# Kernel tuning notes

Measured on AMD Instinct MI355X. Metric: run time of the kernel, lower is better.

Reference implementation:

```python
import jax, jax.numpy as jnp
import numpy as np

N = 200000          # nodes
E = 800000          # edges (avg degree ~4, molecular graphs)
F_IN = 128          # dataset.num_node_features
HID = 32            # hidden_channels -> widths 32, 64, 128
N_TASKS = 128       # dataset.num_tasks
G = 8000            # number of graphs in the batch
EPS = 1e-5


def _glorot(key, shape):
    fan_in, fan_out = shape[0], shape[1]
    lim = np.sqrt(6.0 / (fan_in + fan_out)).astype(np.float32)
    return jax.random.uniform(key, shape, jnp.float32, -lim, lim)


def setup_inputs() -> dict:
    key = jax.random.key(0)
    ks = jax.random.split(key, 16)
    x = jax.random.normal(ks[0], (N, F_IN), jnp.float32)
    edge_index = jax.random.randint(ks[1], (2, E), 0, N, jnp.int64)
    batch = jnp.sort(jax.random.randint(ks[2], (N,), 0, G, jnp.int64))
    return {
        "x": x,
        "edge_index": edge_index,
        "batch": batch,
        "norm_w": jnp.ones((1,), jnp.float32),
        "norm_b": jnp.zeros((1,), jnp.float32),
        "W1": _glorot(ks[3], (F_IN, HID)),
        "b1": jnp.zeros((HID,), jnp.float32),
        "W2": _glorot(ks[4], (HID, 2 * HID)),
        "b2": jnp.zeros((2 * HID,), jnp.float32),
        "W3": _glorot(ks[5], (2 * HID, 4 * HID)),
        "b3": jnp.zeros((4 * HID,), jnp.float32),
        "lin1_W": _glorot(ks[6], (4 * HID, 256)),
        "lin1_b": jnp.zeros((256,), jnp.float32),
        "lin2_W": _glorot(ks[7], (256, N_TASKS)),
        "lin2_b": jnp.zeros((N_TASKS,), jnp.float32),
    }


def _instance_norm(x, batch, w, b):
    # PyG InstanceNorm: per-graph, per-channel mean / biased var, scalar affine.
    ones = jnp.ones((x.shape[0], 1), x.dtype)
    cnt = jnp.maximum(jax.ops.segment_sum(ones, batch, num_segments=G), 1.0)  # [G,1]
    mean = jax.ops.segment_sum(x, batch, num_segments=G) / cnt               # [G,C]
    var = jax.ops.segment_sum(x * x, batch, num_segments=G) / cnt - mean * mean
    xn = (x - mean[batch]) * jax.lax.rsqrt(var[batch] + EPS)
    return xn * w + b


def _gcn_conv(x, src, dst, dis, W, b):
    # GCNConv: h = xW; out_i = sum_j (d_i d_j)^{-1/2} h_j over A+I edges; + bias.
    h = x @ W
    msg = h[src] * (dis[src] * dis[dst])[:, None]          # [E, C] gather
    agg = jax.ops.segment_sum(msg, dst, num_segments=x.shape[0])
    agg = agg + h * (dis * dis)[:, None]                   # self-loop term
    return agg + b


def reference(x, edge_index, batch, norm_w, norm_b, W1, b1, W2, b2, W3, b3,
              lin1_W, lin1_b, lin2_W, lin2_b):
    src, dst = edge_index[0], edge_index[1]
    # degrees on A + I (all edge weights 1)
    deg = 1.0 + jax.ops.segment_sum(jnp.ones((E,), x.dtype), dst, num_segments=N)
    dis = jax.lax.rsqrt(deg)                                # deg >= 1, safe

    h = _instance_norm(x, batch, norm_w, norm_b)
    h = jax.nn.relu(_gcn_conv(h, src, dst, dis, W1, b1))
    h = jax.nn.relu(_gcn_conv(h, src, dst, dis, W2, b2))
    h = jax.nn.relu(_gcn_conv(h, src, dst, dis, W3, b3))

    # global_max_pool; empty graphs -> 0 (values are >=0 post-relu)
    pooled = jnp.maximum(jax.ops.segment_max(h, batch, num_segments=G), 0.0)

    out = jax.nn.relu(pooled @ lin1_W + lin1_b)
    return out @ lin2_W + lin2_b
```

## Files before the change

kernel.cpp:

```cpp
#include <hip/hip_runtime.h>
#include <hip/hip_bf16.h>
#include <stdint.h>

#define NN 200000
#define NE 800000
#define FIN 128
#define NG 8000
#define EPSV 1e-5f
#define NBS ((NN + 255) / 256)

static __device__ __forceinline__ void u2f(uint4 v, float4& lo, float4& hi) {
    lo.x = __uint_as_float(v.x << 16); lo.y = __uint_as_float(v.x & 0xffff0000u);
    lo.z = __uint_as_float(v.y << 16); lo.w = __uint_as_float(v.y & 0xffff0000u);
    hi.x = __uint_as_float(v.z << 16); hi.y = __uint_as_float(v.z & 0xffff0000u);
    hi.z = __uint_as_float(v.w << 16); hi.w = __uint_as_float(v.w & 0xffff0000u);
}
static __device__ __forceinline__ unsigned int pk(float a, float b) {
    __hip_bfloat16 x = __float2bfloat16(a), y = __float2bfloat16(b);
    return (unsigned int)(*(unsigned short*)&x) | ((unsigned int)(*(unsigned short*)&y) << 16);
}

__global__ void k_cnt(const int* __restrict__ dst, int* __restrict__ cnt) {
    int e = blockIdx.x * 256 + threadIdx.x;
    if (e < NE) atomicAdd(&cnt[dst[e]], 1);
}

__global__ void k_blocksum(const int* __restrict__ cnt, int* __restrict__ bsum) {
    __shared__ int sh[256];
    int b = blockIdx.x, t = threadIdx.x;
    int idx = b * 256 + t;
    sh[t] = (idx < NN) ? cnt[idx] : 0;
    __syncthreads();
    for (int o = 128; o > 0; o >>= 1) {
        if (t < o) sh[t] += sh[t + o];
        __syncthreads();
    }
    if (t == 0) bsum[b] = sh[0];
}

__global__ __launch_bounds__(1024) void k_scanb(const int* __restrict__ bsum, int* __restrict__ bpre) {
    __shared__ int sh[1024];
    int t = threadIdx.x;
    int v = (t < NBS) ? bsum[t] : 0;
    sh[t] = v;
    __syncthreads();
    for (int o = 1; o < 1024; o <<= 1) {
        int add = (t >= o) ? sh[t - o] : 0;
        __syncthreads();
        sh[t] += add;
        __syncthreads();
    }
    if (t < NBS) bpre[t] = sh[t] - v;
}

__global__ void k_scanchunk(const int* __restrict__ cnt, const int* __restrict__ bpre,
                            int* __restrict__ rowstart) {
    __shared__ int sh[256];
    int b = blockIdx.x, t = threadIdx.x;
    int idx = b * 256 + t;
    int v = (idx < NN) ? cnt[idx] : 0;
    sh[t] = v;
    __syncthreads();
    for (int o = 1; o < 256; o <<= 1) {
        int add = (t >= o) ? sh[t - o] : 0;
        __syncthreads();
        sh[t] += add;
        __syncthreads();
    }
    if (idx < NN) rowstart[idx] = bpre[b] + sh[t] - v;
    if (idx == 0) rowstart[NN] = NE;
}

__global__ void k_dis(int* __restrict__ cnt) {
    int n = blockIdx.x * 256 + threadIdx.x;
    if (n < NN) {
        float d = rsqrtf(1.0f + (float)cnt[n]);
        ((float*)cnt)[n] = d;
    }
}

__global__ void k_fill(const int* __restrict__ src, const int* __restrict__ dst,
                       int* __restrict__ cursor, int* __restrict__ csr) {
    int e = blockIdx.x * 256 + threadIdx.x;
    if (e < NE) {
        int pos = atomicAdd(&cursor[dst[e]], 1);
        csr[pos] = src[e];
    }
}

__global__ void k_starts(const int* __restrict__ batch, int* __restrict__ startg) {
    int n = blockIdx.x * 256 + threadIdx.x;
    if (n >= NN) return;
    int b = batch[n];
    int prev = (n == 0) ? -1 : batch[n - 1];
    for (int g = prev + 1; g <= b; ++g) startg[g] = n;
    if (n == NN - 1) {
        for (int g = b + 1; g <= NG; ++g) startg[g] = NN;
    }
}

__global__ __launch_bounds__(256) void k_stats2(const float* __restrict__ x,
                                                const int* __restrict__ startg,
                                                const float* __restrict__ nw,
                                                const float* __restrict__ nb,
                                                float* __restrict__ scale,
                                                float* __restrict__ shift) {
    __shared__ float4 rsum[256], rsq[256];
    int g = blockIdx.x;
    int s = startg[g], e = startg[g + 1];
    if (s == e) return;
    int t = threadIdx.x;
    int slot = t >> 5, c4 = t & 31;
    const float4* x4 = (const float4*)x;
    float4 sum = {0.f, 0.f, 0.f, 0.f}, sq = {0.f, 0.f, 0.f, 0.f};
    for (int n = s + slot; n < e; n += 8) {
        float4 v = x4[n * 32 + c4];
        sum.x += v.x; sum.y += v.y; sum.z += v.z; sum.w += v.w;
        sq.x += v.x * v.x; sq.y += v.y * v.y; sq.z += v.z * v.z; sq.w += v.w * v.w;
    }
    rsum[slot * 32 + c4] = sum;
    rsq[slot * 32 + c4] = sq;
    __syncthreads();
    if (t < 32) {
        float4 S = rsum[t], Q = rsq[t];
#pragma unroll
        for (int sl = 1; sl < 8; ++sl) {
            float4 a = rsum[sl * 32 + t], b = rsq[sl * 32 + t];
            S.x += a.x; S.y += a.y; S.z += a.z; S.w += a.w;
            Q.x += b.x; Q.y += b.y; Q.z += b.z; Q.w += b.w;
        }
        float inv = 1.0f / (float)(e - s);
        float w = nw[0], b = nb[0];
        float4 sc, sh;
        {
            float m = S.x * inv, v = fmaxf(Q.x * inv - m * m, 0.f);
            float is = rsqrtf(v + EPSV); sc.x = is * w; sh.x = b - m * is * w;
        }
        {
            float m = S.y * inv, v = fmaxf(Q.y * inv - m * m, 0.f);
            float is = rsqrtf(v + EPSV); sc.y = is * w; sh.y = b - m * is * w;
        }
        {
            float m = S.z * inv, v = fmaxf(Q.z * inv - m * m, 0.f);
            float is = rsqrtf(v + EPSV); sc.z = is * w; sh.z = b - m * is * w;
        }
        {
            float m = S.w * inv, v = fmaxf(Q.w * inv - m * m, 0.f);
            float is = rsqrtf(v + EPSV); sc.w = is * w; sh.w = b - m * is * w;
        }
        ((float4*)scale)[g * 32 + t] = sc;
        ((float4*)shift)[g * 32 + t] = sh;
    }
}

#define SXIDX(n, c4) ((n) * 32 + (((c4) + ((n) >> 1)) & 31))

__global__ __launch_bounds__(256) void k_conv1t(const float* __restrict__ x,
                                                const int* __restrict__ batch,
                                                const float* __restrict__ scale,
                                                const float* __restrict__ shift,
                                                const float* __restrict__ W1,
                                                const float* __restrict__ dis,
                                                float* __restrict__ p1) {
    __shared__ float sW[FIN * 32];
    __shared__ float sx[64 * FIN];
    int t = threadIdx.x;
    const float4* W4 = (const float4*)W1;
    for (int i = t; i < FIN * 32 / 4; i += 256) ((float4*)sW)[i] = W4[i];
    int base = blockIdx.x * 64;
    const float4* x4 = (const float4*)x;
    const float4* sc4 = (const float4*)scale;
    const float4* sh4 = (const float4*)shift;
    for (int i = t; i < 64 * 32; i += 256) {
        int nl = i >> 5, c4 = i & 31;
        int n = base + nl;
        int g = batch[n];
        float4 xv = x4[n * 32 + c4];
        float4 sc = sc4[g * 32 + c4];
        float4 sh = sh4[g * 32 + c4];
        float4 r;
        r.x = xv.x * sc.x + sh.x;
        r.y = xv.y * sc.y + sh.y;
        r.z = xv.z * sc.z + sh.z;
        r.w = xv.w * sc.w + sh.w;
        ((float4*)sx)[SXIDX(nl, c4)] = r;
    }
    __syncthreads();
    int kq = t & 7;
    int n0 = (t >> 3) * 2;
    float4 acc[2];
    acc[0] = {0.f, 0.f, 0.f, 0.f};
    acc[1] = {0.f, 0.f, 0.f, 0.f};
    const float4* sx4 = (const float4*)sx;
    const float4* sW4 = (const float4*)sW;
    for (int c4 = 0; c4 < 32; ++c4) {
        float4 w0 = sW4[(c4 * 4 + 0) * 8 + kq];
        float4 w1 = sW4[(c4 * 4 + 1) * 8 + kq];
        float4 w2 = sW4[(c4 * 4 + 2) * 8 + kq];
        float4 w3 = sW4[(c4 * 4 + 3) * 8 + kq];
#pragma unroll
        for (int i = 0; i < 2; ++i) {
            float4 a = sx4[SXIDX(n0 + i, c4)];
            acc[i].x += a.x * w0.x + a.y * w1.x + a.z * w2.x + a.w * w3.x;
            acc[i].y += a.x * w0.y + a.y * w1.y + a.z * w2.y + a.w * w3.y;
            acc[i].z += a.x * w0.z + a.y * w1.z + a.z * w2.z + a.w * w3.z;
            acc[i].w += a.x * w0.w + a.y * w1.w + a.z * w2.w + a.w * w3.w;
        }
    }
#pragma unroll
    for (int i = 0; i < 2; ++i) {
        int n = base + n0 + i;
        float d = dis[n];
        float4 r;
        r.x = acc[i].x * d; r.y = acc[i].y * d;
        r.z = acc[i].z * d; r.w = acc[i].w * d;
        ((float4*)p1)[n * 8 + kq] = r;
    }
}

__global__ __launch_bounds__(256) void k_gather1(const float* __restrict__ p1,
                                                 const int* __restrict__ rowstart,
                                                 const int* __restrict__ csr,
                                                 const float* __restrict__ dis,
                                                 const float* __restrict__ b1,
                                                 float* __restrict__ p2) {
    int tid = blockIdx.x * 256 + threadIdx.x;
    int n = tid >> 3, c4 = tid & 7;
    const float4* p1_4 = (const float4*)p1;
    int s = rowstart[n], e = rowstart[n + 1];
    float4 agg = p1_4[n * 8 + c4];
    int j = s;
    for (; j + 1 < e; j += 2) {
        float4 v0 = p1_4[csr[j] * 8 + c4];
        float4 v1 = p1_4[csr[j + 1] * 8 + c4];
        agg.x += v0.x + v1.x; agg.y += v0.y + v1.y;
        agg.z += v0.z + v1.z; agg.w += v0.w + v1.w;
    }
    if (j < e) {
        float4 v = p1_4[csr[j] * 8 + c4];
        agg.x += v.x; agg.y += v.y; agg.z += v.z; agg.w += v.w;
    }
    float d = dis[n];
    float4 bb = ((const float4*)b1)[c4];
    float4 r;
    r.x = fmaxf(d * agg.x + bb.x, 0.f) * d;
    r.y = fmaxf(d * agg.y + bb.y, 0.f) * d;
    r.z = fmaxf(d * agg.z + bb.z, 0.f) * d;
    r.w = fmaxf(d * agg.w + bb.w, 0.f) * d;
    ((float4*)p2)[n * 8 + c4] = r;
}

__global__ __launch_bounds__(256) void k_conv2g(const float* __restrict__ p2,
                                                const int* __restrict__ rowstart,
                                                const int* __restrict__ csr,
                                                const float* __restrict__ dis,
                                                const float* __restrict__ W2,
                                                const float* __restrict__ b2v,
                                                __hip_bfloat16* __restrict__ p3h) {
    __shared__ float sW[32 * 64];
    __shared__ float4 spart[16 * 16];
    __shared__ float sa[16 * 32];
    int t = threadIdx.x;
    const float4* W4 = (const float4*)W2;
    for (int i = t; i < 32 * 64 / 4; i += 256) ((float4*)sW)[i] = W4[i];
    int base = blockIdx.x * 16;
    const float4* p2_4 = (const float4*)p2;
    {
        int node = t >> 4, c4 = t & 7, half = (t >> 3) & 1;
        int n = base + node;
        int s = rowstart[n], e = rowstart[n + 1];
        float4 agg = {0.f, 0.f, 0.f, 0.f};
        if (half == 0) {
            agg = p2_4[n * 8 + c4];
            for (int j = s; j < e; j += 2) {
                float4 v = p2_4[csr[j] * 8 + c4];
                agg.x += v.x; agg.y += v.y; agg.z += v.z; agg.w += v.w;
            }
        } else {
            for (int j = s + 1; j < e; j += 2) {
                float4 v = p2_4[csr[j] * 8 + c4];
                agg.x += v.x; agg.y += v.y; agg.z += v.z; agg.w += v.w;
            }
        }
        spart[node * 16 + half * 8 + c4] = agg;
    }
    __syncthreads();
    if (t < 128) {
        int nd = t >> 3, cc = t & 7;
        float4 a = spart[nd * 16 + cc], b = spart[nd * 16 + 8 + cc];
        float d = dis[base + nd];
        float4 r;
        r.x = d * (a.x + b.x); r.y = d * (a.y + b.y);
        r.z = d * (a.z + b.z); r.w = d * (a.w + b.w);
        ((float4*)sa)[nd * 8 + cc] = r;
    }
    __syncthreads();
    int k = t & 63, grp = t >> 6;
    float acc[4] = {0.f, 0.f, 0.f, 0.f};
    for (int c = 0; c < 32; ++c) {
        float w = sW[c * 64 + k];
#pragma unroll
        for (int q = 0; q < 4; ++q) acc[q] += sa[(grp * 4 + q) * 32 + c] * w;
    }
    float bb = b2v[k];
#pragma unroll
    for (int q = 0; q < 4; ++q) {
        int n = base + grp * 4 + q;
        float h = fmaxf(acc[q] + bb, 0.f);
        p3h[n * 64 + k] = __float2bfloat16(h * dis[n]);
    }
}

__global__ __launch_bounds__(256) void k_gather3(const __hip_bfloat16* __restrict__ p3h,
                                                 const int* __restrict__ rowstart,
                                                 const int* __restrict__ csr,
                                                 const float* __restrict__ dis,
                                                 __hip_bfloat16* __restrict__ a3h) {
    int tid = blockIdx.x * 256 + threadIdx.x;
    int n = tid >> 3, c8 = tid & 7;
    const uint4* p3q = (const uint4*)p3h;
    int s = rowstart[n], e = rowstart[n + 1];
    float4 alo, ahi;
    u2f(p3q[n * 8 + c8], alo, ahi);
    int j = s;
    for (; j + 1 < e; j += 2) {
        float4 l0, h0, l1, h1;
        u2f(p3q[csr[j] * 8 + c8], l0, h0);
        u2f(p3q[csr[j + 1] * 8 + c8], l1, h1);
        alo.x += l0.x + l1.x; alo.y += l0.y + l1.y;
        alo.z += l0.z + l1.z; alo.w += l0.w + l1.w;
        ahi.x += h0.x + h1.x; ahi.y += h0.y + h1.y;
        ahi.z += h0.z + h1.z; ahi.w += h0.w + h1.w;
    }
    if (j < e) {
        float4 l0, h0;
        u2f(p3q[csr[j] * 8 + c8], l0, h0);
        alo.x += l0.x; alo.y += l0.y; alo.z += l0.z; alo.w += l0.w;
        ahi.x += h0.x; ahi.y += h0.y; ahi.z += h0.z; ahi.w += h0.w;
    }
    float d = dis[n];
    uint4 o;
    o.x = pk(d * alo.x, d * alo.y);
    o.y = pk(d * alo.z, d * alo.w);
    o.z = pk(d * ahi.x, d * ahi.y);
    o.w = pk(d * ahi.z, d * ahi.w);
    ((uint4*)a3h)[n * 8 + c8] = o;
}

__global__ __launch_bounds__(256) void k_conv3t(const __hip_bfloat16* __restrict__ a3h,
                                                const float* __restrict__ W3,
                                                const float* __restrict__ b3v,
                                                const int* __restrict__ batch,
                                                unsigned int* __restrict__ pooled) {
    __shared__ float sW[64 * 128];
    __shared__ float sa[64 * 64];
    __shared__ int sbatch[64];
    int t = threadIdx.x;
    const float4* W4 = (const float4*)W3;
    for (int i = t; i < 64 * 128 / 4; i += 256) ((float4*)sW)[i] = W4[i];
    int base = blockIdx.x * 64;
    if (t < 64) sbatch[t] = batch[base + t];
    const uint4* a3q = (const uint4*)a3h;
    for (int i = t; i < 64 * 8; i += 256) {
        int nl = i >> 3, c8 = i & 7;
        float4 lo, hi;
        u2f(a3q[(size_t)base * 8 + i], lo, hi);
        ((float4*)sa)[nl * 16 + c8 * 2] = lo;
        ((float4*)sa)[nl * 16 + c8 * 2 + 1] = hi;
    }
    __syncthreads();
    int k0 = (t & 31) * 4;
    int n0 = (t >> 5) * 8;
    float acc[8][4];
#pragma unroll
    for (int i = 0; i < 8; ++i)
#pragma unroll
        for (int j = 0; j < 4; ++j) acc[i][j] = 0.f;
    const float4* sa4 = (const float4*)sa;
    for (int c4 = 0; c4 < 16; ++c4) {
        float4 w0 = *(const float4*)&sW[(c4 * 4 + 0) * 128 + k0];
        float4 w1 = *(const float4*)&sW[(c4 * 4 + 1) * 128 + k0];
        float4 w2 = *(const float4*)&sW[(c4 * 4 + 2) * 128 + k0];
        float4 w3 = *(const float4*)&sW[(c4 * 4 + 3) * 128 + k0];
#pragma unroll
        for (int i = 0; i < 8; ++i) {
            float4 a = sa4[(n0 + i) * 16 + c4];
            acc[i][0] += a.x * w0.x + a.y * w1.x + a.z * w2.x + a.w * w3.x;
            acc[i][1] += a.x * w0.y + a.y * w1.y + a.z * w2.y + a.w * w3.y;
            acc[i][2] += a.x * w0.z + a.y * w1.z + a.z * w2.z + a.w * w3.z;
            acc[i][3] += a.x * w0.w + a.y * w1.w + a.z * w2.w + a.w * w3.w;
        }
    }
    float4 bb = *(const float4*)&b3v[k0];
    float bbv[4] = {bb.x, bb.y, bb.z, bb.w};
    int curg = sbatch[n0];
    float cm[4] = {0.f, 0.f, 0.f, 0.f};
#pragma unroll
    for (int i = 0; i < 8; ++i) {
        int g = sbatch[n0 + i];
        if (g != curg) {
#pragma unroll
            for (int j = 0; j < 4; ++j) {
                atomicMax(&pooled[curg * 128 + k0 + j], __float_as_uint(cm[j]));
                cm[j] = 0.f;
            }
            curg = g;
        }
#pragma unroll
        for (int j = 0; j < 4; ++j)
            cm[j] = fmaxf(cm[j], fmaxf(acc[i][j] + bbv[j], 0.f));
    }
#pragma unroll
    for (int j = 0; j < 4; ++j)
        atomicMax(&pooled[curg * 128 + k0 + j], __float_as_uint(cm[j]));
}

__global__ __launch_bounds__(256) void k_lin1(const float* __restrict__ pooled,
                                              const float* __restrict__ W,
                                              const float* __restrict__ bias,
                                              float* __restrict__ mid) {
    __shared__ float sp[8 * 128];
    int t = threadIdx.x;
    int base = blockIdx.x * 8;
    for (int i = t; i < 8 * 128; i += 256) sp[i] = pooled[base * 128 + i];
    __syncthreads();
    float acc[8] = {0.f, 0.f, 0.f, 0.f, 0.f, 0.f, 0.f, 0.f};
    for (int c = 0; c < 128; ++c) {
        float w = W[c * 256 + t];
#pragma unroll
        for (int gl = 0; gl < 8; ++gl) acc[gl] += sp[gl * 128 + c] * w;
    }
    float bb = bias[t];
#pragma unroll
    for (int gl = 0; gl < 8; ++gl) mid[(base + gl) * 256 + t] = fmaxf(acc[gl] + bb, 0.f);
}

__global__ __launch_bounds__(128) void k_lin2(const float* __restrict__ mid,
                                              const float* __restrict__ W,
                                              const float* __restrict__ bias,
                                              float* __restrict__ out) {
    __shared__ float sm[16 * 256];
    int t = threadIdx.x;
    int base = blockIdx.x * 16;
    for (int i = t; i < 16 * 256; i += 128) sm[i] = mid[base * 256 + i];
    __syncthreads();
    float acc[16];
#pragma unroll
    for (int i = 0; i < 16; ++i) acc[i] = 0.f;
    for (int c = 0; c < 256; ++c) {
        float w = W[c * 128 + t];
#pragma unroll
        for (int gl = 0; gl < 16; ++gl) acc[gl] += sm[gl * 256 + c] * w;
    }
    float bb = bias[t];
#pragma unroll
    for (int gl = 0; gl < 16; ++gl)
        out[(base + gl) * 128 + t] = acc[gl] + bb;
}

extern "C" void kernel_launch(void* const* d_in, const int* in_sizes, int n_in,
                              void* d_out, int out_size, void* d_ws, size_t ws_size,
                              hipStream_t stream) {
    (void)in_sizes; (void)n_in; (void)out_size; (void)ws_size;
    const float* x   = (const float*)d_in[0];
    const int* ei    = (const int*)d_in[1];
    const int* src = ei;
    const int* dst = ei + NE;
    const int* batch = (const int*)d_in[2];
    const float* nw  = (const float*)d_in[3];
    const float* nb  = (const float*)d_in[4];
    const float* W1  = (const float*)d_in[5];
    const float* b1  = (const float*)d_in[6];
    const float* W2  = (const float*)d_in[7];
    const float* b2  = (const float*)d_in[8];
    const float* W3  = (const float*)d_in[9];
    const float* b3  = (const float*)d_in[10];
    const float* l1W = (const float*)d_in[11];
    const float* l1b = (const float*)d_in[12];
    const float* l2W = (const float*)d_in[13];
    const float* l2b = (const float*)d_in[14];
    float* out = (float*)d_out;

    char* wsp = (char*)d_ws;
    int*   cnt      = (int*)wsp;   wsp += (size_t)NN * 4;
    int*   rowstart = (int*)wsp;   wsp += (size_t)(NN + 1) * 4;
    int*   cursor   = (int*)wsp;   wsp += (size_t)NN * 4;
    int*   bsum     = (int*)wsp;   wsp += (size_t)NBS * 4;
    int*   bpre     = (int*)wsp;   wsp += (size_t)NBS * 4;
    int*   startg   = (int*)wsp;   wsp += (size_t)(NG + 1) * 4;
    int*   csr      = (int*)wsp;   wsp += (size_t)NE * 4;
    wsp += ((256 - ((uintptr_t)wsp & 255)) & 255);
    float* scale   = (float*)wsp; wsp += (size_t)NG * 128 * 4;
    float* shift   = (float*)wsp; wsp += (size_t)NG * 128 * 4;
    float* pooled  = (float*)wsp; wsp += (size_t)NG * 128 * 4;
    float* regionA = (float*)wsp; wsp += (size_t)NN * 64 * 4;
    float* regionB = (float*)wsp; wsp += (size_t)NN * 64 * 4;

    float* dis  = (float*)cnt;
    float* p1   = regionA;
    float* p2   = regionA + (size_t)NN * 32;
    __hip_bfloat16* p3h = (__hip_bfloat16*)regionB;
    __hip_bfloat16* a3h = (__hip_bfloat16*)regionA;
    float* mid  = regionB;

    hipMemsetAsync(cnt, 0, (size_t)NN * 4, stream);
    k_cnt<<<(NE + 255) / 256, 256, 0, stream>>>(dst, cnt);
    k_blocksum<<<NBS, 256, 0, stream>>>(cnt, bsum);
    k_scanb<<<1, 1024, 0, stream>>>(bsum, bpre);
    k_scanchunk<<<NBS, 256, 0, stream>>>(cnt, bpre, rowstart);
    k_dis<<<(NN + 255) / 256, 256, 0, stream>>>(cnt);
    hipMemcpyAsync(cursor, rowstart, (size_t)NN * 4, hipMemcpyDeviceToDevice, stream);
    k_fill<<<(NE + 255) / 256, 256, 0, stream>>>(src, dst, cursor, csr);

    k_starts<<<(NN + 255) / 256, 256, 0, stream>>>(batch, startg);
    k_stats2<<<NG, 256, 0, stream>>>(x, startg, nw, nb, scale, shift);
    k_conv1t<<<NN / 64, 256, 0, stream>>>(x, batch, scale, shift, W1, dis, p1);
    k_gather1<<<NN * 8 / 256, 256, 0, stream>>>(p1, rowstart, csr, dis, b1, p2);
    k_conv2g<<<NN / 16, 256, 0, stream>>>(p2, rowstart, csr, dis, W2, b2, p3h);
    k_gather3<<<NN * 8 / 256, 256, 0, stream>>>(p3h, rowstart, csr, dis, a3h);
    hipMemsetAsync(pooled, 0, (size_t)NG * 128 * 4, stream);
    k_conv3t<<<NN / 64, 256, 0, stream>>>(a3h, W3, b3, batch, (unsigned int*)pooled);

    k_lin1<<<NG / 8, 256, 0, stream>>>(pooled, l1W, l1b, mid);
    k_lin2<<<NG / 16, 128, 0, stream>>>(mid, l2W, l2b, out);
}
```

Measured before the change: 545.2 us.

## Read weights via wave-uniform scalar loads in conv1 and conv3 GEMMs

Both dense transform kernels stop staging weights in shared memory. Each lane now owns one node row, and each wave takes a wave-uniform slice of output columns (readfirstlane), so weight reads become uniform loads that can go through the scalar cache. This removes the LDS weight staging and the LDS bandwidth spent on weight reads, and padded LDS rows avoid bank conflicts. Conv3 also stages its results in LDS before the per-graph max pooling. The trade-offs are more accumulator registers per thread and a dependence on the scalar cache for weight bandwidth.

Result: slower. 558.0 us (+2.3%).

```diff
diff --git a/kernel.cpp b/kernel.cpp
--- a/kernel.cpp
+++ b/kernel.cpp
@@ -153,20 +153,15 @@
     }
 }
 
-#define SXIDX(n, c4) ((n) * 32 + (((c4) + ((n) >> 1)) & 31))
-
-__global__ __launch_bounds__(256) void k_conv1t(const float* __restrict__ x,
+__global__ __launch_bounds__(256) void k_conv1s(const float* __restrict__ x,
                                                 const int* __restrict__ batch,
                                                 const float* __restrict__ scale,
                                                 const float* __restrict__ shift,
                                                 const float* __restrict__ W1,
                                                 const float* __restrict__ dis,
                                                 float* __restrict__ p1) {
-    __shared__ float sW[FIN * 32];
-    __shared__ float sx[64 * FIN];
-    int t = threadIdx.x;
-    const float4* W4 = (const float4*)W1;
-    for (int i = t; i < FIN * 32 / 4; i += 256) ((float4*)sW)[i] = W4[i];
+    __shared__ float4 sx4[64 * 33];
+    int t = threadIdx.x;
     int base = blockIdx.x * 64;
     const float4* x4 = (const float4*)x;
     const float4* sc4 = (const float4*)scale;
@@ -179,43 +174,42 @@
         float4 sc = sc4[g * 32 + c4];
         float4 sh = sh4[g * 32 + c4];
         float4 r;
-        r.x = xv.x * sc.x + sh.x;
-        r.y = xv.y * sc.y + sh.y;
-        r.z = xv.z * sc.z + sh.z;
-        r.w = xv.w * sc.w + sh.w;
-        ((float4*)sx)[SXIDX(nl, c4)] = r;
-    }
-    __syncthreads();
-    int kq = t & 7;
-    int n0 = (t >> 3) * 2;
-    float4 acc[2];
-    acc[0] = {0.f, 0.f, 0.f, 0.f};
-    acc[1] = {0.f, 0.f, 0.f, 0.f};
-    const float4* sx4 = (const float4*)sx;
-    const float4* sW4 = (const float4*)sW;
+        r.x = fmaf(xv.x, sc.x, sh.x);
+        r.y = fmaf(xv.y, sc.y, sh.y);
+        r.z = fmaf(xv.z, sc.z, sh.z);
+        r.w = fmaf(xv.w, sc.w, sh.w);
+        sx4[nl * 33 + c4] = r;
+    }
+    __syncthreads();
+    int lane = t & 63;
+    int kq = __builtin_amdgcn_readfirstlane(t >> 6) * 2;
+    const float4* W4 = (const float4*)W1;
+    const float4* arow = &sx4[lane * 33];
+    float4 acc0 = {0.f, 0.f, 0.f, 0.f}, acc1 = {0.f, 0.f, 0.f, 0.f};
+#pragma unroll 4
     for (int c4 = 0; c4 < 32; ++c4) {
-        float4 w0 = sW4[(c4 * 4 + 0) * 8 + kq];
-        float4 w1 = sW4[(c4 * 4 + 1) * 8 + kq];
-        float4 w2 = sW4[(c4 * 4 + 2) * 8 + kq];
-        float4 w3 = sW4[(c4 * 4 + 3) * 8 + kq];
-#pragma unroll
-        for (int i = 0; i < 2; ++i) {
-            float4 a = sx4[SXIDX(n0 + i, c4)];
-            acc[i].x += a.x * w0.x + a.y * w1.x + a.z * w2.x + a.w * w3.x;
-            acc[i].y += a.x * w0.y + a.y * w1.y + a.z * w2.y + a.w * w3.y;
-            acc[i].z += a.x * w0.z + a.y * w1.z + a.z * w2.z + a.w * w3.z;
-            acc[i].w += a.x * w0.w + a.y * w1.w + a.z * w2.w + a.w * w3.w;
-        }
-    }
-#pragma unroll
-    for (int i = 0; i < 2; ++i) {
-        int n = base + n0 + i;
-        float d = dis[n];
-        float4 r;
-        r.x = acc[i].x * d; r.y = acc[i].y * d;
-        r.z = acc[i].z * d; r.w = acc[i].w * d;
-        ((float4*)p1)[n * 8 + kq] = r;
-    }
+        float4 a = arow[c4];
+        int rb = c4 * 32 + kq;
+        float4 wA0 = W4[rb +  0], wA1 = W4[rb +  1];
+        float4 wB0 = W4[rb +  8], wB1 = W4[rb +  9];
+        float4 wC0 = W4[rb + 16], wC1 = W4[rb + 17];
+        float4 wD0 = W4[rb + 24], wD1 = W4[rb + 25];
+        acc0.x += a.x * wA0.x + a.y * wB0.x + a.z * wC0.x + a.w * wD0.x;
+        acc0.y += a.x * wA0.y + a.y * wB0.y + a.z * wC0.y + a.w * wD0.y;
+        acc0.z += a.x * wA0.z + a.y * wB0.z + a.z * wC0.z + a.w * wD0.z;
+        acc0.w += a.x * wA0.w + a.y * wB0.w + a.z * wC0.w + a.w * wD0.w;
+        acc1.x += a.x * wA1.x + a.y * wB1.x + a.z * wC1.x + a.w * wD1.x;
+        acc1.y += a.x * wA1.y + a.y * wB1.y + a.z * wC1.y + a.w * wD1.y;
+        acc1.z += a.x * wA1.z + a.y * wB1.z + a.z * wC1.z + a.w * wD1.z;
+        acc1.w += a.x * wA1.w + a.y * wB1.w + a.z * wC1.w + a.w * wD1.w;
+    }
+    int n = base + lane;
+    float d = dis[n];
+    float4 r0, r1;
+    r0.x = acc0.x * d; r0.y = acc0.y * d; r0.z = acc0.z * d; r0.w = acc0.w * d;
+    r1.x = acc1.x * d; r1.y = acc1.y * d; r1.z = acc1.z * d; r1.w = acc1.w * d;
+    ((float4*)p1)[n * 8 + kq] = r0;
+    ((float4*)p1)[n * 8 + kq + 1] = r1;
 }
 
 __global__ __launch_bounds__(256) void k_gather1(const float* __restrict__ p1,
@@ -347,72 +341,85 @@
     ((uint4*)a3h)[n * 8 + c8] = o;
 }
 
-__global__ __launch_bounds__(256) void k_conv3t(const __hip_bfloat16* __restrict__ a3h,
+__global__ __launch_bounds__(256) void k_conv3s(const __hip_bfloat16* __restrict__ a3h,
                                                 const float* __restrict__ W3,
                                                 const float* __restrict__ b3v,
                                                 const int* __restrict__ batch,
                                                 unsigned int* __restrict__ pooled) {
-    __shared__ float sW[64 * 128];
-    __shared__ float sa[64 * 64];
+    __shared__ uint4 sa[64 * 9];
+    __shared__ float sp[64 * 132];
     __shared__ int sbatch[64];
     int t = threadIdx.x;
-    const float4* W4 = (const float4*)W3;
-    for (int i = t; i < 64 * 128 / 4; i += 256) ((float4*)sW)[i] = W4[i];
     int base = blockIdx.x * 64;
     if (t < 64) sbatch[t] = batch[base + t];
     const uint4* a3q = (const uint4*)a3h;
     for (int i = t; i < 64 * 8; i += 256) {
-        int nl = i >> 3, c8 = i & 7;
+        sa[(i >> 3) * 9 + (i & 7)] = a3q[(size_t)base * 8 + i];
+    }
+    __syncthreads();
+    int lane = t & 63;
+    int kq = __builtin_amdgcn_readfirstlane(t >> 6) * 8;
+    const float4* W4 = (const float4*)W3;
+    const uint4* arow = &sa[lane * 9];
+    float4 acc[8];
+#pragma unroll
+    for (int j = 0; j < 8; ++j) acc[j] = {0.f, 0.f, 0.f, 0.f};
+#pragma unroll 2
+    for (int q = 0; q < 8; ++q) {
         float4 lo, hi;
-        u2f(a3q[(size_t)base * 8 + i], lo, hi);
-        ((float4*)sa)[nl * 16 + c8 * 2] = lo;
-        ((float4*)sa)[nl * 16 + c8 * 2 + 1] = hi;
-    }
-    __syncthreads();
-    int k0 = (t & 31) * 4;
-    int n0 = (t >> 5) * 8;
-    float acc[8][4];
-#pragma unroll
-    for (int i = 0; i < 8; ++i)
-#pragma unroll
-        for (int j = 0; j < 4; ++j) acc[i][j] = 0.f;
-    const float4* sa4 = (const float4*)sa;
-    for (int c4 = 0; c4 < 16; ++c4) {
-        float4 w0 = *(const float4*)&sW[(c4 * 4 + 0) * 128 + k0];
-        float4 w1 = *(const float4*)&sW[(c4 * 4 + 1) * 128 + k0];
-        float4 w2 = *(const float4*)&sW[(c4 * 4 + 2) * 128 + k0];
-        float4 w3 = *(const float4*)&sW[(c4 * 4 + 3) * 128 + k0];
-#pragma unroll
-        for (int i = 0; i < 8; ++i) {
-            float4 a = sa4[(n0 + i) * 16 + c4];
-            acc[i][0] += a.x * w0.x + a.y * w1.x + a.z * w2.x + a.w * w3.x;
-            acc[i][1] += a.x * w0.y + a.y * w1.y + a.z * w2.y + a.w * w3.y;
-            acc[i][2] += a.x * w0.z + a.y * w1.z + a.z * w2.z + a.w * w3.z;
-            acc[i][3] += a.x * w0.w + a.y * w1.w + a.z * w2.w + a.w * w3.w;
-        }
-    }
-    float4 bb = *(const float4*)&b3v[k0];
-    float bbv[4] = {bb.x, bb.y, bb.z, bb.w};
+        u2f(arow[q], lo, hi);
+        float av[8] = {lo.x, lo.y, lo.z, lo.w, hi.x, hi.y, hi.z, hi.w};
+#pragma unroll
+        for (int r = 0; r < 8; ++r) {
+            float ar = av[r];
+            int rb = (q * 8 + r) * 32 + kq;
+#pragma unroll
+            for (int j = 0; j < 8; ++j) {
+                float4 wv = W4[rb + j];
+                acc[j].x += ar * wv.x;
+                acc[j].y += ar * wv.y;
+                acc[j].z += ar * wv.z;
+                acc[j].w += ar * wv.w;
+            }
+        }
+    }
+    const float4* B4 = (const float4*)b3v;
+    float* sprow = &sp[lane * 132];
+#pragma unroll
+    for (int j = 0; j < 8; ++j) {
+        float4 bb = B4[kq + j];
+        float4 h;
+        h.x = fmaxf(acc[j].x + bb.x, 0.f);
+        h.y = fmaxf(acc[j].y + bb.y, 0.f);
+        h.z = fmaxf(acc[j].z + bb.z, 0.f);
+        h.w = fmaxf(acc[j].w + bb.w, 0.f);
+        *(float4*)&sprow[(kq + j) * 4] = h;
+    }
+    __syncthreads();
+    int k4 = t & 31, n0 = (t >> 5) * 8;
     int curg = sbatch[n0];
-    float cm[4] = {0.f, 0.f, 0.f, 0.f};
-#pragma unroll
-    for (int i = 0; i < 8; ++i) {
-        int g = sbatch[n0 + i];
+    float4 cm = {0.f, 0.f, 0.f, 0.f};
+#pragma unroll
+    for (int ii = 0; ii < 8; ++ii) {
+        int g = sbatch[n0 + ii];
+        float4 h = *(const float4*)&sp[(n0 + ii) * 132 + k4 * 4];
         if (g != curg) {
-#pragma unroll
-            for (int j = 0; j < 4; ++j) {
-                atomicMax(&pooled[curg * 128 + k0 + j], __float_as_uint(cm[j]));
-                cm[j] = 0.f;
-            }
+            atomicMax(&pooled[curg * 128 + k4 * 4 + 0], __float_as_uint(cm.x));
+            atomicMax(&pooled[curg * 128 + k4 * 4 + 1], __float_as_uint(cm.y));
+            atomicMax(&pooled[curg * 128 + k4 * 4 + 2], __float_as_uint(cm.z));
+            atomicMax(&pooled[curg * 128 + k4 * 4 + 3], __float_as_uint(cm.w));
+            cm = {0.f, 0.f, 0.f, 0.f};
             curg = g;
         }
-#pragma unroll
-        for (int j = 0; j < 4; ++j)
-            cm[j] = fmaxf(cm[j], fmaxf(acc[i][j] + bbv[j], 0.f));
-    }
-#pragma unroll
-    for (int j = 0; j < 4; ++j)
-        atomicMax(&pooled[curg * 128 + k0 + j], __float_as_uint(cm[j]));
+        cm.x = fmaxf(cm.x, h.x);
+        cm.y = fmaxf(cm.y, h.y);
+        cm.z = fmaxf(cm.z, h.z);
+        cm.w = fmaxf(cm.w, h.w);
+    }
+    atomicMax(&pooled[curg * 128 + k4 * 4 + 0], __float_as_uint(cm.x));
+    atomicMax(&pooled[curg * 128 + k4 * 4 + 1], __float_as_uint(cm.y));
+    atomicMax(&pooled[curg * 128 + k4 * 4 + 2], __float_as_uint(cm.z));
+    atomicMax(&pooled[curg * 128 + k4 * 4 + 3], __float_as_uint(cm.w));
 }
 
 __global__ __launch_bounds__(256) void k_lin1(const float* __restrict__ pooled,
@@ -514,12 +521,12 @@
 
     k_starts<<<(NN + 255) / 256, 256, 0, stream>>>(batch, startg);
     k_stats2<<<NG, 256, 0, stream>>>(x, startg, nw, nb, scale, shift);
-    k_conv1t<<<NN / 64, 256, 0, stream>>>(x, batch, scale, shift, W1, dis, p1);
+    k_conv1s<<<NN / 64, 256, 0, stream>>>(x, batch, scale, shift, W1, dis, p1);
     k_gather1<<<NN * 8 / 256, 256, 0, stream>>>(p1, rowstart, csr, dis, b1, p2);
     k_conv2g<<<NN / 16, 256, 0, stream>>>(p2, rowstart, csr, dis, W2, b2, p3h);
     k_gather3<<<NN * 8 / 256, 256, 0, stream>>>(p3h, rowstart, csr, dis, a3h);
     hipMemsetAsync(pooled, 0, (size_t)NG * 128 * 4, stream);
-    k_conv3t<<<NN / 64, 256, 0, stream>>>(a3h, W3, b3, batch, (unsigned int*)pooled);
+    k_conv3s<<<NN / 64, 256, 0, stream>>>(a3h, W3, b3, batch, (unsigned int*)pooled);
 
     k_lin1<<<NG / 8, 256, 0, stream>>>(pooled, l1W, l1b, mid);
     k_lin2<<<NG / 16, 128, 0, stream>>>(mid, l2W, l2b, out);
```
